# Kernel optimization log

Measured on AMD Instinct MI355X. Metric: run time of the kernel, lower is better.

The kernel has to match this reference:

```python
import jax, jax.numpy as jnp
import numpy as np

B, IN_SEQ, TGT_SEQ = 128, 50, 25
IN_SIZE, OUT_SIZE, RNN = 128, 128, 2048


def setup_inputs() -> dict:
    key = jax.random.key(0)
    ks = jax.random.split(key, 10)
    s_in = 1.0 / np.sqrt(IN_SIZE)
    s_out = 1.0 / np.sqrt(OUT_SIZE)
    s_rnn = 1.0 / np.sqrt(RNN)
    return {
        "encoder_inputs": jax.random.normal(ks[0], (B, IN_SEQ, IN_SIZE), jnp.float32),
        "decoder_inputs": jax.random.normal(ks[1], (B, TGT_SEQ, IN_SIZE), jnp.float32),
        "fc1_w": jax.random.uniform(ks[2], (OUT_SIZE, IN_SIZE), jnp.float32, -s_in, s_in),
        "fc1_b": jax.random.uniform(ks[3], (OUT_SIZE,), jnp.float32, -s_in, s_in),
        "w_ih": jax.random.uniform(ks[4], (3 * RNN, OUT_SIZE), jnp.float32, -s_rnn, s_rnn),
        "w_hh": jax.random.uniform(ks[5], (3 * RNN, RNN), jnp.float32, -s_rnn, s_rnn),
        "b_ih": jax.random.uniform(ks[6], (3 * RNN,), jnp.float32, -s_rnn, s_rnn),
        "b_hh": jax.random.uniform(ks[7], (3 * RNN,), jnp.float32, -s_rnn, s_rnn),
        "fc2_w": jax.random.uniform(ks[8], (OUT_SIZE, RNN), jnp.float32, -s_rnn, s_rnn),
        "fc2_b": jax.random.uniform(ks[9], (OUT_SIZE,), jnp.float32, -s_rnn, s_rnn),
    }


def _gru_cell(x, h, w_ih, w_hh, b_ih, b_hh):
    # PyTorch GRUCell: gates ordered (r, z, n)
    gi = x @ w_ih.T + b_ih            # [B, 3R]
    gh = h @ w_hh.T + b_hh            # [B, 3R]
    i_r, i_z, i_n = jnp.split(gi, 3, axis=-1)
    h_r, h_z, h_n = jnp.split(gh, 3, axis=-1)
    r = jax.nn.sigmoid(i_r + h_r)
    z = jax.nn.sigmoid(i_z + h_z)
    n = jnp.tanh(i_n + r * h_n)
    return (1.0 - z) * n + z * h


def reference(encoder_inputs, decoder_inputs, fc1_w, fc1_b, w_ih, w_hh, b_ih, b_hh, fc2_w, fc2_b):
    # Eval mode: F.dropout(training=False) is identity.
    enc = encoder_inputs @ fc1_w.T + fc1_b              # [B, S_in, OUT]
    enc_t = jnp.transpose(enc, (1, 0, 2))               # time-major [S_in, B, OUT]
    h0 = jnp.zeros((encoder_inputs.shape[0], RNN), enc.dtype)

    def enc_step(state, x):
        return _gru_cell(x, state, w_ih, w_hh, b_ih, b_hh), None

    state, _ = jax.lax.scan(enc_step, h0, enc_t[:-1])   # input_seq - 1 steps

    def dec_step(carry, _):
        state, inp = carry
        inp = jax.lax.stop_gradient(inp)                # inp.detach()
        state = _gru_cell(inp, state, w_ih, w_hh, b_ih, b_hh)
        out = inp + state @ fc2_w.T + fc2_b             # residual decoder
        return (state, out), out

    _, outs = jax.lax.scan(dec_step, (state, enc_t[-1]), None, length=TGT_SEQ)
    return jnp.transpose(outs, (1, 0, 2))               # [B, TGT_SEQ, OUT]
```

## Files before the change

kernel.cpp:

```cpp
#include <hip/hip_runtime.h>
#include <limits.h>

constexpr int kB   = 128;
constexpr int kSin = 50;
constexpr int kT   = 25;
constexpr int kD   = 128;
constexpr int kR   = 2048;
constexpr int kNB  = 256;
constexpr int kNT  = 512;

typedef __bf16 bf16x8 __attribute__((ext_vector_type(8)));
typedef float  f32x4  __attribute__((ext_vector_type(4)));
typedef unsigned short u16;
typedef unsigned long long u64;

__device__ __forceinline__ float bf2f(u16 u){ union{unsigned i; float f;}x; x.i=((unsigned)u)<<16; return x.f; }
__device__ __forceinline__ u16 f2bf(float f){ union{float f; unsigned i;}x; x.f=f; return (u16)((x.i + 0x7FFFu + ((x.i>>16)&1u))>>16); }
__device__ __forceinline__ float sigm(float x){ return 1.f/(1.f+__expf(-x)); }

__device__ __forceinline__ void stg32(unsigned* p, unsigned v){
    __hip_atomic_store(p, v, __ATOMIC_RELAXED, __HIP_MEMORY_SCOPE_AGENT);
}
__device__ __forceinline__ void stg64(u64* p, u64 v){
    __hip_atomic_store(p, v, __ATOMIC_RELAXED, __HIP_MEMORY_SCOPE_AGENT);
}

__device__ __forceinline__ bf16x8 pack8(float4 a, float4 b){
    union{ bf16x8 v; u16 u[8]; } t;
    t.u[0]=f2bf(a.x); t.u[1]=f2bf(a.y); t.u[2]=f2bf(a.z); t.u[3]=f2bf(a.w);
    t.u[4]=f2bf(b.x); t.u[5]=f2bf(b.y); t.u[6]=f2bf(b.z); t.u[7]=f2bf(b.w);
    return t.v;
}

__device__ __forceinline__ void gbar(int* flags, int* genp, int k)
{
    __syncthreads();
    const int tid = threadIdx.x, wg = blockIdx.x;
    if (tid == 0) atomicMax(&flags[wg*16], k);
    if (wg == 0 && tid < 64) {
        const int i0 = tid * 4;
        for (;;) {
            int a = atomicMax(&flags[(i0+0)*16], INT_MIN);
            int b = atomicMax(&flags[(i0+1)*16], INT_MIN);
            int c = atomicMax(&flags[(i0+2)*16], INT_MIN);
            int d = atomicMax(&flags[(i0+3)*16], INT_MIN);
            if (__ballot((a>=k)&&(b>=k)&&(c>=k)&&(d>=k)) == ~0ull) break;
            __builtin_amdgcn_s_sleep(1);
        }
        atomicMax(&genp[tid*16], k);
    }
    if (tid == 0) {
        if (wg != 0)
            while (atomicMax(&genp[(wg&63)*16], INT_MIN) < k) __builtin_amdgcn_s_sleep(1);
        __builtin_amdgcn_fence(__ATOMIC_ACQUIRE, "agent");
    }
    __syncthreads();
}

__device__ __forceinline__ void cvt_f32_bf16(const float* __restrict__ s, u16* __restrict__ d,
                                             int n4, int gtid, int gstride)
{
    for (int i = gtid; i < n4; i += gstride) {
        float4 v = ((const float4*)s)[i];
        u64 pk = (u64)f2bf(v.x) | ((u64)f2bf(v.y)<<16) | ((u64)f2bf(v.z)<<32) | ((u64)f2bf(v.w)<<48);
        stg64((u64*)d + i, pk);
    }
}

template<int NT, int NACC>
__device__ __forceinline__ void small_gemm(
    const u16* __restrict__ Am, int alda,
    const u16* __restrict__ Bp, int bldb,
    f32x4 (&acc)[NACC], u16* pool)
{
    const int tid=threadIdx.x, lane=tid&63, wv=tid>>6, g=wv>>2, mt=wv&3, ar=lane&15, aq=lane>>4;
    u16* sA = pool;
    u16* sB = pool + 8704;
    { int q=tid,     r=q>>4, c=q&15; *(uint4*)&sA[r*136+c*8] = *(const uint4*)(Am + r*alda + c*8); }
    { int q=tid+512, r=q>>4, c=q&15; *(uint4*)&sA[r*136+c*8] = *(const uint4*)(Am + r*alda + c*8); }
    for (int q=tid; q<NT*256; q+=kNT){
        int r=q>>4, c=q&15;
        *(uint4*)&sB[r*136+c*8] = *(const uint4*)(Bp + (size_t)r*bldb + c*8);
    }
    __syncthreads();
#pragma unroll
    for (int jt=0; jt<NT; ++jt){
        if ((jt&1) != g) continue;
#pragma unroll
        for (int kk=0; kk<4; ++kk){
            bf16x8 a = *(const bf16x8*)&sA[(mt*16+ar)*136 + kk*32 + aq*8];
            bf16x8 b = *(const bf16x8*)&sB[(jt*16+ar)*136 + kk*32 + aq*8];
            acc[jt>>1] = __builtin_amdgcn_mfma_f32_16x16x32_bf16(a,b,acc[jt>>1],0,0,0);
        }
    }
    __syncthreads();
}

__device__ __forceinline__ void gru_phase_reg(
    const u16* __restrict__ hcur, u16* __restrict__ hnxt,
    const u16* __restrict__ xb,
    const bf16x8 (&wB)[3][8], const bf16x8 (&wI)[3],
    const float4 b4, float (&hprev)[4],
    int wgc, int mrow0, u16* smem, u16* sH)
{
    const int tid=threadIdx.x, lane=tid&63, w=tid>>6, ar=lane&15, aq=lane>>4;
    const f32x4 zz = {0.f,0.f,0.f,0.f};
    f32x4 acc[3][4] = {{zz,zz,zz,zz},{zz,zz,zz,zz},{zz,zz,zz,zz}};
    f32x4 xn[4] = {zz,zz,zz,zz};

#pragma unroll
    for (int mt=0; mt<4; ++mt){
        const int row = mrow0 + mt*16 + ar;
        bf16x8 af[8];
#pragma unroll
        for (int c=0; c<8; ++c){
            const int s = 16*w + 2*c + (aq>>1);
            af[c] = *(const bf16x8*)(hcur + (((s*128 + row)<<4) + (aq&1)*8));
        }
#pragma unroll
        for (int c=0; c<8; ++c){
            acc[0][mt] = __builtin_amdgcn_mfma_f32_16x16x32_bf16(af[c], wB[0][c], acc[0][mt],0,0,0);
            acc[1][mt] = __builtin_amdgcn_mfma_f32_16x16x32_bf16(af[c], wB[1][c], acc[1][mt],0,0,0);
            acc[2][mt] = __builtin_amdgcn_mfma_f32_16x16x32_bf16(af[c], wB[2][c], acc[2][mt],0,0,0);
        }
    }
    if (w < 4){
#pragma unroll
        for (int mt=0; mt<4; ++mt){
            bf16x8 ax = *(const bf16x8*)(xb + (mrow0+mt*16+ar)*kD + 32*w + aq*8);
            acc[0][mt] = __builtin_amdgcn_mfma_f32_16x16x32_bf16(ax, wI[0], acc[0][mt],0,0,0);
            acc[1][mt] = __builtin_amdgcn_mfma_f32_16x16x32_bf16(ax, wI[1], acc[1][mt],0,0,0);
            xn[mt]     = __builtin_amdgcn_mfma_f32_16x16x32_bf16(ax, wI[2], xn[mt],0,0,0);
        }
    }
    float* red = (float*)smem;
#define RCELL(wp,g4,mt) (red + (((((wp)*4+(g4))*4+(mt))*64 + lane)<<2))
    if (w >= 4){
#pragma unroll
        for (int g=0; g<3; ++g)
#pragma unroll
            for (int mt=0; mt<4; ++mt)
                *(f32x4*)RCELL(w-4, g, mt) = acc[g][mt];
    }
    __syncthreads();
    if (w < 4){
#pragma unroll
        for (int g=0; g<3; ++g)
#pragma unroll
            for (int mt=0; mt<4; ++mt)
                acc[g][mt] += *(f32x4*)RCELL(w, g, mt);
#pragma unroll
        for (int g=0; g<3; ++g)
#pragma unroll
            for (int mt=0; mt<4; ++mt)
                *(f32x4*)RCELL(w, g, mt) = acc[g][mt];
#pragma unroll
        for (int mt=0; mt<4; ++mt)
            *(f32x4*)RCELL(w, 3, mt) = xn[mt];
    }
    __syncthreads();
    if (tid < 256){
        const int mt = tid>>6, ls = tid&63, aqs = ls>>4, ars = ls&15;
        f32x4 R=zz, Z=zz, NH=zz, NX=zz;
#pragma unroll
        for (int wp=0; wp<4; ++wp){
            R  += *(f32x4*)(red + ((((wp*4+0)*4+mt)*64 + ls)<<2));
            Z  += *(f32x4*)(red + ((((wp*4+1)*4+mt)*64 + ls)<<2));
            NH += *(f32x4*)(red + ((((wp*4+2)*4+mt)*64 + ls)<<2));
            NX += *(f32x4*)(red + ((((wp*4+3)*4+mt)*64 + ls)<<2));
        }
#pragma unroll
        for (int rr=0; rr<4; ++rr){
            const int m = mrow0 + mt*16 + aqs*4 + rr;
            float r_ = sigm(R[rr] + b4.x);
            float z_ = sigm(Z[rr] + b4.y);
            float n_ = tanhf(NX[rr] + b4.z + r_*(NH[rr] + b4.w));
            float hn = (1.f-z_)*n_ + z_*hprev[rr];
            hprev[rr] = hn;
            u16 hb = f2bf(hn);
            sH[(mt*16 + aqs*4 + rr)*16 + ars] = hb;
            unsigned other = (unsigned)__shfl_xor((int)(unsigned)hb, 1);
            if (!(ars&1))
                stg32((unsigned*)(hnxt + ((wgc*128+m)<<4) + ars), (unsigned)hb | (other<<16));
        }
    }
#undef RCELL
    __syncthreads();
}

__device__ __forceinline__ void fc2_partial(
    const u16* __restrict__ sH, const bf16x8 (&wF2)[4],
    int wgc, int mh, float* __restrict__ part)
{
    const int tid=threadIdx.x, lane=tid&63, w=tid>>6, ar=lane&15, aq=lane>>4;
    const int mt = w&3, nh = w>>2;
    bf16x8 a;
    if (aq < 2) a = *(const bf16x8*)&sH[(mt*16+ar)*16 + aq*8];
    else {
#pragma unroll
        for (int i=0;i<8;++i) a[i] = (__bf16)0.f;
    }
    const f32x4 zz = {0.f,0.f,0.f,0.f};
    f32x4 acc[4] = {zz,zz,zz,zz};
#pragma unroll
    for (int j=0;j<4;++j)
        acc[j] = __builtin_amdgcn_mfma_f32_16x16x32_bf16(a, wF2[j], acc[j],0,0,0);
#pragma unroll
    for (int j=0;j<4;++j){
        const int col = (nh*4+j)*16 + ar;
#pragma unroll
        for (int rr=0;rr<4;++rr){
            const int row = mt*16 + aq*4 + rr;
            stg32((unsigned*)(part + ((((size_t)mh*64+row)*128 + wgc)*128 + col)),
                  __float_as_uint(acc[j][rr]));
        }
    }
}

__global__ __launch_bounds__(kNT, 2) void seq2seq_kernel(
    const void* __restrict__ enc_in_raw, const void* __restrict__ fc1_w_raw,
    const void* __restrict__ fc1_b_raw,  const void* __restrict__ w_ih_raw,
    const void* __restrict__ w_hh_raw,   const void* __restrict__ b_ih_raw,
    const void* __restrict__ b_hh_raw,   const void* __restrict__ fc2_w_raw,
    const void* __restrict__ fc2_b_raw,
    void* __restrict__ out_raw,
    u16* __restrict__ enc_act,
    u16* __restrict__ h_b16,
    u16* __restrict__ inp_b16,
    float* __restrict__ inp_f32,
    float* __restrict__ encF,
    float* __restrict__ bias,
    float* __restrict__ part,
    int* flags, int* genp,
    u16* __restrict__ cv_encx, u16* __restrict__ cv_fc2, u16* __restrict__ cv_fc1)
{
    __shared__ __align__(16) u16 smem[33792];
    __shared__ int sflag;
    u16* sH = smem + 32768;
    const int wg = blockIdx.x, tid = threadIdx.x;
    const int wgc = wg & 127, mrow0 = (wg >> 7) * 64;
    const int lane = tid & 63, wv = tid >> 6, ar = lane & 15, aq = lane >> 4;
    const int gtid = wg * kNT + tid, gstride = kNB * kNT;
    int tok = 1;

    {
        const u16* p = (const u16*)enc_in_raw;
        int found = 0;
        for (int i = tid; i < 16384; i += kNT) found |= ((p[i] & 0x7F80) == 0x7F80) ? 1 : 0;
        if (tid == 0) sflag = 0;
        __syncthreads();
        if (found) sflag = 1;
        __syncthreads();
    }
    const bool F32 = (sflag != 0);

    bf16x8 wB[3][8];
    bf16x8 wI[3];
    {
        const int w4 = wv & 3;
        if (F32){
            const float* Wh = (const float*)w_hh_raw;
            const float* Wi = (const float*)w_ih_raw;
#pragma unroll
            for (int g=0; g<3; ++g)
#pragma unroll
                for (int c=0; c<8; ++c){
                    size_t o = (size_t)(g*kR + wgc*16 + ar)*kR + 256*wv + 32*c + aq*8;
                    wB[g][c] = pack8(*(const float4*)(Wh+o), *(const float4*)(Wh+o+4));
                }
#pragma unroll
            for (int g=0; g<3; ++g){
                size_t o = (size_t)(g*kR + wgc*16 + ar)*kD + 32*w4 + aq*8;
                wI[g] = pack8(*(const float4*)(Wi+o), *(const float4*)(Wi+o+4));
            }
        } else {
            const u16* Wh = (const u16*)w_hh_raw;
            const u16* Wi = (const u16*)w_ih_raw;
#pragma unroll
            for (int g=0; g<3; ++g)
#pragma unroll
                for (int c=0; c<8; ++c)
                    wB[g][c] = *(const bf16x8*)(Wh + (size_t)(g*kR + wgc*16 + ar)*kR + 256*wv + 32*c + aq*8);
#pragma unroll
            for (int g=0; g<3; ++g)
                wI[g] = *(const bf16x8*)(Wi + (size_t)(g*kR + wgc*16 + ar)*kD + 32*w4 + aq*8);
        }
    }

    if (F32) {
        cvt_f32_bf16((const float*)fc2_w_raw, cv_fc2,  (kD*kR)/4,       gtid, gstride);
        cvt_f32_bf16((const float*)fc1_w_raw, cv_fc1,  (kD*kD)/4,       gtid, gstride);
        cvt_f32_bf16((const float*)enc_in_raw,cv_encx, (kB*kSin*kD)/4,  gtid, gstride);
        for (int i = gtid; i < 3*kR; i += gstride) {
            stg32((unsigned*)&bias[i],        __float_as_uint(((const float*)b_ih_raw)[i]));
            stg32((unsigned*)&bias[3*kR + i], __float_as_uint(((const float*)b_hh_raw)[i]));
        }
        for (int i = gtid; i < kD; i += gstride) {
            stg32((unsigned*)&bias[6*kR + i],      __float_as_uint(((const float*)fc1_b_raw)[i]));
            stg32((unsigned*)&bias[6*kR + kD + i], __float_as_uint(((const float*)fc2_b_raw)[i]));
        }
    } else {
        for (int i = gtid; i < 3*kR; i += gstride) {
            stg32((unsigned*)&bias[i],        __float_as_uint(bf2f(((const u16*)b_ih_raw)[i])));
            stg32((unsigned*)&bias[3*kR + i], __float_as_uint(bf2f(((const u16*)b_hh_raw)[i])));
        }
        for (int i = gtid; i < kD; i += gstride) {
            stg32((unsigned*)&bias[6*kR + i],      __float_as_uint(bf2f(((const u16*)fc1_b_raw)[i])));
            stg32((unsigned*)&bias[6*kR + kD + i], __float_as_uint(bf2f(((const u16*)fc2_b_raw)[i])));
        }
    }
    for (int i = gtid; i < (kB*kR)/2; i += gstride) stg32((unsigned*)h_b16 + i, 0u);
    gbar(flags, genp, tok++);

    const u16* ENCX = F32 ? cv_encx : (const u16*)enc_in_raw;
    const u16* WF2  = F32 ? cv_fc2  : (const u16*)fc2_w_raw;
    const u16* WF1  = F32 ? cv_fc1  : (const u16*)fc1_w_raw;

    float4 b4;
    {
        const int hc = wgc*16 + ar;
        b4.x = bias[hc]      + bias[3*kR+hc];
        b4.y = bias[kR+hc]   + bias[4*kR+hc];
        b4.z = bias[2*kR+hc];
        b4.w = bias[5*kR+hc];
    }
    bf16x8 wF2[4];
    {
        const int nh = wv>>2;
#pragma unroll
        for (int j=0;j<4;++j){
            if (aq < 2)
                wF2[j] = *(const bf16x8*)(WF2 + (size_t)((nh*4+j)*16+ar)*kR + wgc*16 + aq*8);
            else {
#pragma unroll
                for (int i=0;i<8;++i) wF2[j][i] = (__bf16)0.f;
            }
        }
    }
    const float fc2b = bias[6*kR + kD + (wg&1)*64 + (tid&63)];
    float hprev[4] = {0.f, 0.f, 0.f, 0.f};

    if (wgc < kSin) {
        const int g = wv>>2, mt = wv&3;
        const f32x4 zz = {0.f,0.f,0.f,0.f};
        f32x4 ae[4] = {zz,zz,zz,zz};
        small_gemm<8,4>(ENCX + ((size_t)mrow0*kSin + wgc)*kD, kSin*kD, WF1, kD, ae, smem);
#pragma unroll
        for (int jt=0; jt<8; ++jt){
            if ((jt&1) != g) continue;
            int col = jt*16 + ar;
            float fb = bias[6*kR + col];
#pragma unroll
            for (int rr=0; rr<4; ++rr){
                int m = mrow0 + mt*16 + aq*4 + rr;
                float v = ae[jt>>1][rr] + fb;
                u16 hb = f2bf(v);
                unsigned other = (unsigned)__shfl_xor((int)(unsigned)hb, 1);
                if (!(ar&1))
                    stg32((unsigned*)(enc_act + ((size_t)wgc*kB + m)*kD + col),
                          (unsigned)hb | (other<<16));
                if (wgc == kSin-1)
                    stg32((unsigned*)(encF + (size_t)m*kD + col), __float_as_uint(v));
            }
        }
    }
    gbar(flags, genp, tok++);

    int par = 0;
    for (int t = 0; t < kSin-1; ++t) {
        gru_phase_reg(h_b16 + (size_t)par*kB*kR, h_b16 + (size_t)(1-par)*kB*kR,
                      enc_act + (size_t)t*kB*kD, wB, wI, b4, hprev, wgc, mrow0, smem, sH);
        gbar(flags, genp, tok++);
        par ^= 1;
    }

    const u16*   ib  = enc_act + (size_t)(kSin-1)*kB*kD;
    const float* ifp = encF;
    const int mh = wg >> 7;
    for (int d = 0; d < kT; ++d) {
        gru_phase_reg(h_b16 + (size_t)par*kB*kR, h_b16 + (size_t)(1-par)*kB*kR,
                      ib, wB, wI, b4, hprev, wgc, mrow0, smem, sH);
        fc2_partial(sH, wF2, wgc, mh, part);
        gbar(flags, genp, tok++);
        par ^= 1;

        u16*   nib = inp_b16 + (size_t)(d&1)*kB*kD;
        float* nif = inp_f32 + (size_t)(d&1)*kB*kD;
        {
            const int row = wg >> 1, ch = wg & 1;
            const int mh2 = row >> 6, rl = row & 63;
            const float* pr = part + (size_t)((mh2*64 + rl)*128)*128;
            const int cl = tid & 63, sg = tid >> 6;
            float s = 0.f;
#pragma unroll
            for (int j=0;j<16;++j) s += pr[(size_t)(sg*16+j)*128 + ch*64 + cl];
            float* red2 = (float*)smem;
            red2[sg*64 + cl] = s;
            __syncthreads();
            if (tid < 64){
                float t2 = 0.f;
#pragma unroll
                for (int g2=0; g2<8; ++g2) t2 += red2[g2*64 + tid];
                const int colg = ch*64 + tid;
                const float o = t2 + fc2b + ifp[(size_t)row*kD + colg];
                const size_t ob = ((size_t)row*kT + d)*kD + colg;
                if (F32) ((float*)out_raw)[ob] = o;
                else     ((u16*)out_raw)[ob]   = f2bf(o);
                stg32((unsigned*)(nif + (size_t)row*kD + colg), __float_as_uint(o));
                u16 hb = f2bf(o);
                unsigned other = (unsigned)__shfl_xor((int)(unsigned)hb, 1);
                if (!(tid&1))
                    stg32((unsigned*)(nib + (size_t)row*kD + colg), (unsigned)hb | (other<<16));
            }
        }
        gbar(flags, genp, tok++);
        ib = nib; ifp = nif;
    }
}

extern "C" void kernel_launch(void* const* d_in, const int* in_sizes, int n_in,
                              void* d_out, int out_size, void* d_ws, size_t ws_size,
                              hipStream_t stream)
{
    size_t off = 0;
    char* ws = (char*)d_ws;
    auto alloc = [&](size_t bytes) -> char* {
        char* p = ws + off;
        off = (off + bytes + 255) & ~(size_t)255;
        return p;
    };
    u16*   enc_act = (u16*)alloc((size_t)kSin*kB*kD*2);
    u16*   h_b16   = (u16*)alloc((size_t)2*kB*kR*2);
    u16*   inp_b16 = (u16*)alloc((size_t)2*kB*kD*2);
    float* inp_f32 = (float*)alloc((size_t)2*kB*kD*4);
    float* encF    = (float*)alloc((size_t)kB*kD*4);
    float* bias    = (float*)alloc((size_t)(6*kR + 2*kD)*4);
    float* part    = (float*)alloc((size_t)2*64*128*128*4);
    int*   flags   = (int*)alloc((size_t)kNB*16*4);
    int*   genp    = (int*)alloc((size_t)64*16*4);
    u16*   cv_encx = (u16*)alloc((size_t)kB*kSin*kD*2);
    u16*   cv_fc2  = (u16*)alloc((size_t)kD*kR*2);
    u16*   cv_fc1  = (u16*)alloc((size_t)kD*kD*2);
    (void)ws_size; (void)in_sizes; (void)n_in; (void)out_size;

    seq2seq_kernel<<<dim3(kNB), dim3(kNT), 0, stream>>>(
        d_in[0], d_in[2], d_in[3], d_in[4], d_in[5], d_in[6], d_in[7], d_in[8], d_in[9],
        d_out,
        enc_act, h_b16, inp_b16, inp_f32, encF, bias, part, flags, genp,
        cv_encx, cv_fc2, cv_fc1);
}
```

Before: 1.643 ms.

## Decentralize grid barrier into per-batch-half domains polled by every block

Replaces the two-level grid barrier (block 0 gathers all flags, then broadcasts through generation slots) with one where every block's first wave polls the flags of its own domain. A domain is the 128 blocks sharing a batch half, and polling uses cheap relaxed loads, with an atomic RMW only every 32nd iteration. The acquire fence is dropped, so loads of data shared between blocks (hidden state, inputs, partial sums, biases) become agent-scope relaxed atomic loads that bypass stale cache lines. This cuts the barrier's critical path and removes cross-half coupling. In exchange, each 128-bit load is split into two 64-bit atomic loads and polling traffic rises, and the ordering guarantees are weaker than an explicit acquire fence.

```diff
diff --git a/kernel.cpp b/kernel.cpp
--- a/kernel.cpp
+++ b/kernel.cpp
@@ -24,6 +24,21 @@
 __device__ __forceinline__ void stg64(u64* p, u64 v){
     __hip_atomic_store(p, v, __ATOMIC_RELAXED, __HIP_MEMORY_SCOPE_AGENT);
 }
+__device__ __forceinline__ unsigned ald32(const void* p){
+    return __hip_atomic_load((const unsigned*)p, __ATOMIC_RELAXED, __HIP_MEMORY_SCOPE_AGENT);
+}
+__device__ __forceinline__ u64 ald64(const void* p){
+    return __hip_atomic_load((const u64*)p, __ATOMIC_RELAXED, __HIP_MEMORY_SCOPE_AGENT);
+}
+__device__ __forceinline__ bf16x8 ald128bf(const u16* p){
+    union{ u64 q[2]; bf16x8 v; } t;
+    t.q[0] = ald64(p);
+    t.q[1] = ald64(p + 4);
+    return t.v;
+}
+__device__ __forceinline__ float aldf(const float* p){
+    union{ unsigned u; float f; } t; t.u = ald32(p); return t.f;
+}
 
 __device__ __forceinline__ bf16x8 pack8(float4 a, float4 b){
     union{ bf16x8 v; u16 u[8]; } t;
@@ -32,27 +47,26 @@
     return t.v;
 }
 
-__device__ __forceinline__ void gbar(int* flags, int* genp, int k)
-{
-    __syncthreads();
-    const int tid = threadIdx.x, wg = blockIdx.x;
-    if (tid == 0) atomicMax(&flags[wg*16], k);
-    if (wg == 0 && tid < 64) {
-        const int i0 = tid * 4;
+__device__ __forceinline__ void gbar(int* flags, int k, int base, int perlane)
+{
+    __syncthreads();
+    const int tid = threadIdx.x;
+    if (tid == 0) atomicMax(&flags[blockIdx.x*16], k);
+    if (tid < 64) {
+        int iter = 0;
         for (;;) {
-            int a = atomicMax(&flags[(i0+0)*16], INT_MIN);
-            int b = atomicMax(&flags[(i0+1)*16], INT_MIN);
-            int c = atomicMax(&flags[(i0+2)*16], INT_MIN);
-            int d = atomicMax(&flags[(i0+3)*16], INT_MIN);
-            if (__ballot((a>=k)&&(b>=k)&&(c>=k)&&(d>=k)) == ~0ull) break;
+            bool ok = true;
+            for (int j = 0; j < perlane; ++j) {
+                const int idx = base + tid*perlane + j;
+                int v;
+                if ((iter & 31) == 31) v = atomicMax(&flags[idx*16], INT_MIN);
+                else                   v = (int)ald32(&flags[idx*16]);
+                ok &= (v >= k);
+            }
+            if (__ballot(ok) == ~0ull) break;
+            ++iter;
             __builtin_amdgcn_s_sleep(1);
         }
-        atomicMax(&genp[tid*16], k);
-    }
-    if (tid == 0) {
-        if (wg != 0)
-            while (atomicMax(&genp[(wg&63)*16], INT_MIN) < k) __builtin_amdgcn_s_sleep(1);
-        __builtin_amdgcn_fence(__ATOMIC_ACQUIRE, "agent");
     }
     __syncthreads();
 }
@@ -115,7 +129,7 @@
 #pragma unroll
         for (int c=0; c<8; ++c){
             const int s = 16*w + 2*c + (aq>>1);
-            af[c] = *(const bf16x8*)(hcur + (((s*128 + row)<<4) + (aq&1)*8));
+            af[c] = ald128bf(hcur + (((s*128 + row)<<4) + (aq&1)*8));
         }
 #pragma unroll
         for (int c=0; c<8; ++c){
@@ -127,7 +141,7 @@
     if (w < 4){
 #pragma unroll
         for (int mt=0; mt<4; ++mt){
-            bf16x8 ax = *(const bf16x8*)(xb + (mrow0+mt*16+ar)*kD + 32*w + aq*8);
+            bf16x8 ax = ald128bf(xb + (mrow0+mt*16+ar)*kD + 32*w + aq*8);
             acc[0][mt] = __builtin_amdgcn_mfma_f32_16x16x32_bf16(ax, wI[0], acc[0][mt],0,0,0);
             acc[1][mt] = __builtin_amdgcn_mfma_f32_16x16x32_bf16(ax, wI[1], acc[1][mt],0,0,0);
             xn[mt]     = __builtin_amdgcn_mfma_f32_16x16x32_bf16(ax, wI[2], xn[mt],0,0,0);
@@ -231,7 +245,7 @@
     float* __restrict__ encF,
     float* __restrict__ bias,
     float* __restrict__ part,
-    int* flags, int* genp,
+    int* flags,
     u16* __restrict__ cv_encx, u16* __restrict__ cv_fc2, u16* __restrict__ cv_fc1)
 {
     __shared__ __align__(16) u16 smem[33792];
@@ -241,6 +255,7 @@
     const int wgc = wg & 127, mrow0 = (wg >> 7) * 64;
     const int lane = tid & 63, wv = tid >> 6, ar = lane & 15, aq = lane >> 4;
     const int gtid = wg * kNT + tid, gstride = kNB * kNT;
+    const int dom = (wg >> 7) * 128;
     int tok = 1;
 
     {
@@ -310,7 +325,7 @@
         }
     }
     for (int i = gtid; i < (kB*kR)/2; i += gstride) stg32((unsigned*)h_b16 + i, 0u);
-    gbar(flags, genp, tok++);
+    gbar(flags, tok++, 0, 4);
 
     const u16* ENCX = F32 ? cv_encx : (const u16*)enc_in_raw;
     const u16* WF2  = F32 ? cv_fc2  : (const u16*)fc2_w_raw;
@@ -319,10 +334,10 @@
     float4 b4;
     {
         const int hc = wgc*16 + ar;
-        b4.x = bias[hc]      + bias[3*kR+hc];
-        b4.y = bias[kR+hc]   + bias[4*kR+hc];
-        b4.z = bias[2*kR+hc];
-        b4.w = bias[5*kR+hc];
+        b4.x = aldf(&bias[hc])      + aldf(&bias[3*kR+hc]);
+        b4.y = aldf(&bias[kR+hc])   + aldf(&bias[4*kR+hc]);
+        b4.z = aldf(&bias[2*kR+hc]);
+        b4.w = aldf(&bias[5*kR+hc]);
     }
     bf16x8 wF2[4];
     {
@@ -330,14 +345,14 @@
 #pragma unroll
         for (int j=0;j<4;++j){
             if (aq < 2)
-                wF2[j] = *(const bf16x8*)(WF2 + (size_t)((nh*4+j)*16+ar)*kR + wgc*16 + aq*8);
+                wF2[j] = ald128bf(WF2 + (size_t)((nh*4+j)*16+ar)*kR + wgc*16 + aq*8);
             else {
 #pragma unroll
                 for (int i=0;i<8;++i) wF2[j][i] = (__bf16)0.f;
             }
         }
     }
-    const float fc2b = bias[6*kR + kD + (wg&1)*64 + (tid&63)];
+    const float fc2b = aldf(&bias[6*kR + kD + (wg&1)*64 + (tid&63)]);
     float hprev[4] = {0.f, 0.f, 0.f, 0.f};
 
     if (wgc < kSin) {
@@ -349,7 +364,7 @@
         for (int jt=0; jt<8; ++jt){
             if ((jt&1) != g) continue;
             int col = jt*16 + ar;
-            float fb = bias[6*kR + col];
+            float fb = aldf(&bias[6*kR + col]);
 #pragma unroll
             for (int rr=0; rr<4; ++rr){
                 int m = mrow0 + mt*16 + aq*4 + rr;
@@ -364,13 +379,13 @@
             }
         }
     }
-    gbar(flags, genp, tok++);
+    gbar(flags, tok++, dom, 2);
 
     int par = 0;
     for (int t = 0; t < kSin-1; ++t) {
         gru_phase_reg(h_b16 + (size_t)par*kB*kR, h_b16 + (size_t)(1-par)*kB*kR,
                       enc_act + (size_t)t*kB*kD, wB, wI, b4, hprev, wgc, mrow0, smem, sH);
-        gbar(flags, genp, tok++);
+        gbar(flags, tok++, dom, 2);
         par ^= 1;
     }
 
@@ -381,7 +396,7 @@
         gru_phase_reg(h_b16 + (size_t)par*kB*kR, h_b16 + (size_t)(1-par)*kB*kR,
                       ib, wB, wI, b4, hprev, wgc, mrow0, smem, sH);
         fc2_partial(sH, wF2, wgc, mh, part);
-        gbar(flags, genp, tok++);
+        gbar(flags, tok++, dom, 2);
         par ^= 1;
 
         u16*   nib = inp_b16 + (size_t)(d&1)*kB*kD;
@@ -393,7 +408,7 @@
             const int cl = tid & 63, sg = tid >> 6;
             float s = 0.f;
 #pragma unroll
-            for (int j=0;j<16;++j) s += pr[(size_t)(sg*16+j)*128 + ch*64 + cl];
+            for (int j=0;j<16;++j) s += aldf(&pr[(size_t)(sg*16+j)*128 + ch*64 + cl]);
             float* red2 = (float*)smem;
             red2[sg*64 + cl] = s;
             __syncthreads();
@@ -402,7 +417,7 @@
 #pragma unroll
                 for (int g2=0; g2<8; ++g2) t2 += red2[g2*64 + tid];
                 const int colg = ch*64 + tid;
-                const float o = t2 + fc2b + ifp[(size_t)row*kD + colg];
+                const float o = t2 + fc2b + aldf(&ifp[(size_t)row*kD + colg]);
                 const size_t ob = ((size_t)row*kT + d)*kD + colg;
                 if (F32) ((float*)out_raw)[ob] = o;
                 else     ((u16*)out_raw)[ob]   = f2bf(o);
@@ -413,7 +428,7 @@
                     stg32((unsigned*)(nib + (size_t)row*kD + colg), (unsigned)hb | (other<<16));
             }
         }
-        gbar(flags, genp, tok++);
+        gbar(flags, tok++, dom, 2);
         ib = nib; ifp = nif;
     }
 }
@@ -437,7 +452,6 @@
     float* bias    = (float*)alloc((size_t)(6*kR + 2*kD)*4);
     float* part    = (float*)alloc((size_t)2*64*128*128*4);
     int*   flags   = (int*)alloc((size_t)kNB*16*4);
-    int*   genp    = (int*)alloc((size_t)64*16*4);
     u16*   cv_encx = (u16*)alloc((size_t)kB*kSin*kD*2);
     u16*   cv_fc2  = (u16*)alloc((size_t)kD*kR*2);
     u16*   cv_fc1  = (u16*)alloc((size_t)kD*kD*2);
@@ -446,6 +460,6 @@
     seq2seq_kernel<<<dim3(kNB), dim3(kNT), 0, stream>>>(
         d_in[0], d_in[2], d_in[3], d_in[4], d_in[5], d_in[6], d_in[7], d_in[8], d_in[9],
         d_out,
-        enc_act, h_b16, inp_b16, inp_f32, encF, bias, part, flags, genp,
+        enc_act, h_b16, inp_b16, inp_f32, encF, bias, part, flags,
         cv_encx, cv_fc2, cv_fc1);
 }
```

Result: faster. 1.583 ms (-3.6%).
